# Optimization experiments

Measured on AMD Instinct MI355X. Metric: run time of the kernel, lower is better.

## Reference

```python
import jax, jax.numpy as jnp
import numpy as np

NC, NF = 64, 16
Z_NEAR, Z_FAR = 2.0, 6.0
EPS = 1e-5


def volume_integral(z_vals, sigmas, radiances):
    # z_vals/sigmas: (B,R,Z,1), radiances: (B,R,Z,F)
    d = z_vals[..., 1:, :] - z_vals[..., :-1, :]
    dists = jnp.concatenate([d, d[..., -1:, :]], axis=-2)            # (B,R,Z,1)
    alpha = 1.0 - jnp.exp(-jax.nn.relu(sigmas) * dists)
    alpha_shifted = jnp.concatenate(
        [jnp.ones_like(alpha[..., :1, :]), 1.0 - alpha + 1e-10], axis=-2)
    Ts = jnp.cumprod(alpha_shifted, axis=-2)                         # transmittance
    weights = alpha * Ts[..., :-1, :]                                # (B,R,Z,1)
    rgb = jnp.sum(weights * radiances, axis=-2)                      # (B,R,F)
    depth = jnp.sum(weights * z_vals, axis=-2)                       # (B,R,1)
    return rgb, depth, weights


def sample_pdf(bins, weights, u, eps=EPS):
    # bins: (N, S+1), weights: (N, S), u: (N, Nf) in [0,1)
    weights = weights + eps
    pdf = weights / jnp.sum(weights, -1, keepdims=True)
    cdf = jnp.cumsum(pdf, -1)
    cdf = jnp.concatenate([jnp.zeros_like(cdf[:, :1]), cdf], -1)     # (N, S+1)
    inds = jax.vmap(jnp.searchsorted)(cdf, u)                        # side='left' == torch default
    below = jnp.clip(inds - 1, 0, None)
    above = jnp.minimum(inds, weights.shape[-1])
    cdf_g0 = jnp.take_along_axis(cdf, below, 1)
    cdf_g1 = jnp.take_along_axis(cdf, above, 1)
    bins_g0 = jnp.take_along_axis(bins, below, 1)
    bins_g1 = jnp.take_along_axis(bins, above, 1)
    denom = cdf_g1 - cdf_g0
    denom = jnp.where(denom < eps, 1.0, denom)
    return bins_g0 + (u - cdf_g0) / denom * (bins_g1 - bins_g0)


def _render(ros, rds, w_sigma, w_feat, u):
    B, R, _ = ros.shape

    def rad(pts):
        return pts @ w_sigma, jax.nn.sigmoid(pts @ w_feat)

    # coarse stratified samples (lindisp=False)
    zl = jnp.linspace(0.0, 1.0, NC, dtype=ros.dtype)
    z_vals = Z_NEAR + (Z_FAR - Z_NEAR) * zl                          # (NC,)
    z_vals = jnp.broadcast_to(z_vals[None, None, :, None], (B, R, NC, 1))
    pts = ros[:, :, None, :] + rds[:, :, None, :] * z_vals           # (B,R,NC,3)
    sigma, feats = rad(pts)

    # coarse pass + importance resampling (no grad in original)
    _, _, weights = volume_integral(z_vals, sigma, feats)
    weights = jax.lax.stop_gradient(weights).reshape(B * R, NC)
    t = z_vals.reshape(B * R, NC)
    tm = 0.5 * (t[:, :-1] + t[:, 1:])                                # (N, NC-1)
    t_pdf = sample_pdf(tm, weights[:, 1:-1], u)                      # (N, NF)
    t_pdf = jax.lax.stop_gradient(t_pdf).reshape(B, R, NF)

    pts_fine = ros[:, :, None, :] + rds[:, :, None, :] * t_pdf[..., None]
    pts_all = jnp.concatenate([pts, pts_fine], axis=-2)              # (B,R,NC+NF,3)
    sigma_all, feats_all = rad(pts_all)

    # merge-sort coarse+fine by depth and gather
    z_all = jnp.concatenate([z_vals, t_pdf[..., None]], axis=-2)     # (B,R,Z,1)
    idx = jnp.argsort(z_all, axis=-2)
    z_all = jnp.take_along_axis(z_all, idx, axis=-2)
    sigma_all = jnp.take_along_axis(sigma_all, idx, axis=-2)
    feats_all = jnp.take_along_axis(
        feats_all, jnp.broadcast_to(idx, feats_all.shape), axis=-2)

    rgb, depth, weights = volume_integral(z_all, sigma_all, feats_all)
    return rgb, depth, weights


def setup_inputs() -> dict:
    key = jax.random.key(0)
    k = jax.random.split(key, 5)
    B, R = 8, 16384
    return {
        "ros": jax.random.normal(k[0], (B, R, 3), jnp.float32),
        "rds": jax.random.normal(k[1], (B, R, 3), jnp.float32),
        "w_sigma": jax.random.normal(k[2], (3, 1), jnp.float32),
        "w_feat": jax.random.normal(k[3], (3, 3), jnp.float32),
        "u": jax.random.uniform(k[4], (B * R, NF), jnp.float32),
    }


def reference(ros, rds, w_sigma, w_feat, u):
    return _render(ros, rds, w_sigma, w_feat, u)
```

## Files before the change

### kernel.cpp

```cpp
#include <hip/hip_runtime.h>

#define NCC 64
#define NFF 16
#define NZ  80
#define BLK 128
#define SLOTS 63

__device__ __forceinline__ float zc_of(int i) {
    return fmaf(4.0f, (float)i * (1.0f / 63.0f), 2.0f);
}
__device__ __forceinline__ float tm_of(int i) {
    return 0.5f * (zc_of(i) + zc_of(i + 1));
}
__device__ __forceinline__ float fast_rcp(float x) { return __builtin_amdgcn_rcpf(x); }

__global__ void __launch_bounds__(BLK, 2)
VolumeRenderer_16192026706363_kernel(const float* __restrict__ ros,
                                     const float* __restrict__ rds,
                                     const float* __restrict__ w_sigma,
                                     const float* __restrict__ w_feat,
                                     const float* __restrict__ u,
                                     float* __restrict__ out,
                                     int nrays)
{
    __shared__ float lds[BLK * SLOTS];
    const int tid = threadIdx.x;
    const int n = blockIdx.x * BLK + tid;
    float* my = &lds[tid * SLOTS];

    const float4* u4p = reinterpret_cast<const float4*>(u + (size_t)n * 16);
    float4 uq0 = u4p[0], uq1 = u4p[1], uq2 = u4p[2], uq3 = u4p[3];

    const float ro0 = ros[n * 3 + 0], ro1 = ros[n * 3 + 1], ro2 = ros[n * 3 + 2];
    const float rd0 = rds[n * 3 + 0], rd1 = rds[n * 3 + 1], rd2 = rds[n * 3 + 2];
    const float s0 = w_sigma[0], s1 = w_sigma[1], s2 = w_sigma[2];
    const float sgA = ro0 * s0 + ro1 * s1 + ro2 * s2;
    const float sgB = rd0 * s0 + rd1 * s1 + rd2 * s2;
    float fA[3], fB[3];
#pragma unroll
    for (int c = 0; c < 3; c++) {
        fA[c] = ro0 * w_feat[0 * 3 + c] + ro1 * w_feat[1 * 3 + c] + ro2 * w_feat[2 * 3 + c];
        fB[c] = rd0 * w_feat[0 * 3 + c] + rd1 * w_feat[1 * 3 + c] + rd2 * w_feat[2 * 3 + c];
    }

    const float LOG2E = 1.4426950408889634f;
    const float DIST  = 4.0f / 63.0f;
    const float K1    = -DIST * LOG2E;

    float T = 1.0f, cum = 0.0f;
    my[0] = 0.0f;
    {
        float e = exp2f(fmaxf(sgA + sgB * 2.0f, 0.0f) * K1);
        T = e + 1e-10f;
    }
    for (int i = 1; i <= 62; i++) {
        float sg = fmaf(sgB, zc_of(i), sgA);
        float e = exp2f(fmaxf(sg, 0.0f) * K1);
        float w = (1.0f - e) * T;
        cum += w + 1e-5f;
        my[i] = cum;
        T *= (e + 1e-10f);
    }
    const float S = cum;
    const float invS = 1.0f / S;

    float tv[16];
#pragma unroll
    for (int q = 0; q < 16; q++) {
        float uu;
        {
            float4 uq = (q < 4) ? uq0 : (q < 8) ? uq1 : (q < 12) ? uq2 : uq3;
            int r = q & 3;
            uu = (r == 0) ? uq.x : (r == 1) ? uq.y : (r == 2) ? uq.z : uq.w;
        }
        float us = uu * S;
        int lo = 0, hi = 63;
#pragma unroll
        for (int s = 0; s < 6; s++) {
            int mid = (lo + hi) >> 1;
            bool lt = (my[mid] < us);
            lo = lt ? mid + 1 : lo;
            hi = lt ? hi : mid;
        }
        int ind = lo;
        int below = (ind - 1 > 0) ? ind - 1 : 0;
        int above = (ind < 62) ? ind : 62;
        float c0 = my[below] * invS, c1 = my[above] * invS;
        float b0 = tm_of(below);
        float denom = c1 - c0;
        denom = (denom < 1e-5f) ? 1.0f : denom;
        float db = (4.0f / 63.0f) * (float)(above - below);
        tv[q] = fmaf((uu - c0) / denom, db, b0);
    }

#pragma unroll
    for (int k = 2; k <= 16; k <<= 1) {
#pragma unroll
        for (int j = k >> 1; j > 0; j >>= 1) {
#pragma unroll
            for (int i = 0; i < 16; i++) {
                int l = i ^ j;
                if (l > i) {
                    float a = tv[i], b = tv[l];
                    float mn = fminf(a, b), mx = fmaxf(a, b);
                    bool up = ((i & k) == 0);
                    tv[i] = up ? mn : mx;
                    tv[l] = up ? mx : mn;
                }
            }
        }
    }
#pragma unroll
    for (int i = 0; i < 16; i++) my[i] = tv[i];

    int ic = 0, jf = 0;
    float zch = 2.0f;
    float zfh = my[0];
    float T2 = 1.0f, acc0 = 0.0f, acc1 = 0.0f, acc2 = 0.0f, accd = 0.0f;

    auto pop = [&]() -> float {
        bool takeC = (zch <= zfh);
        float r = takeC ? zch : zfh;
        if (takeC) { ic++; zch = (ic < NCC) ? zc_of(ic) : 3.0e38f; }
        else       { jf++; zfh = (jf < NFF) ? my[jf] : 3.0e38f; }
        return r;
    };

    auto proc = [&](float z, float d) -> float {
        float sg = fmaf(sgB, z, sgA);
        float e = exp2f(fmaxf(sg, 0.0f) * d * (-LOG2E));
        float alpha = 1.0f - e;
        float w = alpha * T2;
        T2 *= (e + 1e-10f);
        float f0 = fast_rcp(1.0f + exp2f(fmaf(fB[0], z, fA[0]) * (-LOG2E)));
        float f1 = fast_rcp(1.0f + exp2f(fmaf(fB[1], z, fA[1]) * (-LOG2E)));
        float f2 = fast_rcp(1.0f + exp2f(fmaf(fB[2], z, fA[2]) * (-LOG2E)));
        acc0 = fmaf(w, f0, acc0);
        acc1 = fmaf(w, f1, acc1);
        acc2 = fmaf(w, f2, acc2);
        accd = fmaf(w, z, accd);
        return w;
    };

    float* wptr = out + (size_t)nrays * 4 + (size_t)n * NZ;
    float zprev = pop();
    float dlast = 0.0f;
    float wq[4];

    for (int g = 0; g < 19; g++) {
#pragma unroll
        for (int j = 0; j < 4; j++) {
            float z = pop();
            wq[j] = proc(zprev, z - zprev);
            zprev = z;
        }
        *reinterpret_cast<float4*>(wptr + g * 4) =
            make_float4(wq[0], wq[1], wq[2], wq[3]);
    }
#pragma unroll
    for (int j = 0; j < 3; j++) {
        float z = pop();
        dlast = z - zprev;
        wq[j] = proc(zprev, dlast);
        zprev = z;
    }
    wq[3] = proc(zprev, dlast);
    *reinterpret_cast<float4*>(wptr + 19 * 4) =
        make_float4(wq[0], wq[1], wq[2], wq[3]);

    out[(size_t)n * 3 + 0] = acc0;
    out[(size_t)n * 3 + 1] = acc1;
    out[(size_t)n * 3 + 2] = acc2;
    out[(size_t)nrays * 3 + n] = accd;
}

extern "C" void kernel_launch(void* const* d_in, const int* in_sizes, int n_in,
                              void* d_out, int out_size, void* d_ws, size_t ws_size,
                              hipStream_t stream) {
    const float* ros = (const float*)d_in[0];
    const float* rds = (const float*)d_in[1];
    const float* w_sigma = (const float*)d_in[2];
    const float* w_feat = (const float*)d_in[3];
    const float* u = (const float*)d_in[4];
    float* out = (float*)d_out;

    int nrays = in_sizes[0] / 3;
    int grid = nrays / BLK;
    VolumeRenderer_16192026706363_kernel<<<grid, BLK, 0, stream>>>(
        ros, rds, w_sigma, w_feat, u, out, nrays);
}
```

Measured before the change: 107.6 us.

## Replace serial scans and merge with register prefix scans and scatter-based merge

Swaps the serial transmittance and CDF recurrences for fully unrolled blocked prefix-product and prefix-sum scans held in registers, which shortens the dependency chains. The branchy coarse/fine merge loop is replaced by scattering each fine sample into an LDS slot computed from its coarse bin, followed by a branchless fill of the 80 sorted depths. The final pass then computes weights as differences of the prefix products and splits accumulation across two accumulator sets. Block size drops to 64 with a 79-float LDS stride. The large unrolled register arrays (g, c, z, pp) risk high VGPR pressure and spills, and the prefix-product form changes rounding slightly.

```diff
diff --git a/kernel.cpp b/kernel.cpp
--- a/kernel.cpp
+++ b/kernel.cpp
@@ -1,18 +1,68 @@
 #include <hip/hip_runtime.h>
 
+#define BLK 64
+#define STRIDE 79
 #define NCC 64
 #define NFF 16
 #define NZ  80
-#define BLK 128
-#define SLOTS 63
-
-__device__ __forceinline__ float zc_of(int i) {
-    return fmaf(4.0f, (float)i * (1.0f / 63.0f), 2.0f);
-}
-__device__ __forceinline__ float tm_of(int i) {
-    return 0.5f * (zc_of(i) + zc_of(i + 1));
-}
+
 __device__ __forceinline__ float fast_rcp(float x) { return __builtin_amdgcn_rcpf(x); }
+
+template<int N>
+__device__ __forceinline__ void prefix_mul(float* x) {
+#pragma unroll
+    for (int c = 0; c < N; c += 8) {
+#pragma unroll
+        for (int i = 1; i < 8; i++)
+            if (c + i < N) x[c + i] *= x[c + i - 1];
+    }
+    constexpr int G = (N + 7) / 8;
+    float t[G];
+#pragma unroll
+    for (int g = 0; g < G; g++) {
+        int e = 8 * g + 7; if (e > N - 1) e = N - 1;
+        t[g] = x[e];
+    }
+#pragma unroll
+    for (int sh = 1; sh < G; sh <<= 1) {
+#pragma unroll
+        for (int g = G - 1; g >= sh; --g) t[g] *= t[g - sh];
+    }
+#pragma unroll
+    for (int g = 1; g < G; g++) {
+#pragma unroll
+        for (int i = 0; i < 8; i++)
+            if (8 * g + i < N) x[8 * g + i] *= t[g - 1];
+    }
+}
+
+template<int N>
+__device__ __forceinline__ void prefix_add(float* x) {
+#pragma unroll
+    for (int c = 0; c < N; c += 8) {
+#pragma unroll
+        for (int i = 1; i < 8; i++)
+            if (c + i < N) x[c + i] += x[c + i - 1];
+    }
+    constexpr int G = (N + 7) / 8;
+    float t[G];
+#pragma unroll
+    for (int g = 0; g < G; g++) {
+        int e = 8 * g + 7; if (e > N - 1) e = N - 1;
+        t[g] = x[e];
+    }
+#pragma unroll
+    for (int sh = 1; sh < G; sh <<= 1) {
+#pragma unroll
+        for (int g = G - 1; g >= sh; --g) t[g] += t[g - sh];
+    }
+#pragma unroll
+    for (int g = 1; g < G; g++) {
+#pragma unroll
+        for (int i = 0; i < 8; i++)
+            if (8 * g + i < N) x[8 * g + i] += t[g - 1];
+    }
+}
 
 __global__ void __launch_bounds__(BLK, 2)
 VolumeRenderer_16192026706363_kernel(const float* __restrict__ ros,
@@ -23,17 +73,22 @@
                                      float* __restrict__ out,
                                      int nrays)
 {
-    __shared__ float lds[BLK * SLOTS];
+    __shared__ float lds[BLK * STRIDE];
     const int tid = threadIdx.x;
     const int n = blockIdx.x * BLK + tid;
-    float* my = &lds[tid * SLOTS];
+    float* my = &lds[tid * STRIDE];
+
+    const float LOG2E = 1.4426950408889634f;
+    const float NEGL2E = -LOG2E;
+    const float DIST = 4.0f / 63.0f;
+    const float K1 = -DIST * LOG2E;
 
     const float4* u4p = reinterpret_cast<const float4*>(u + (size_t)n * 16);
     float4 uq0 = u4p[0], uq1 = u4p[1], uq2 = u4p[2], uq3 = u4p[3];
-
     const float ro0 = ros[n * 3 + 0], ro1 = ros[n * 3 + 1], ro2 = ros[n * 3 + 2];
     const float rd0 = rds[n * 3 + 0], rd1 = rds[n * 3 + 1], rd2 = rds[n * 3 + 2];
     const float s0 = w_sigma[0], s1 = w_sigma[1], s2 = w_sigma[2];
+
     const float sgA = ro0 * s0 + ro1 * s1 + ro2 * s2;
     const float sgB = rd0 * s0 + rd1 * s1 + rd2 * s2;
     float fA[3], fB[3];
@@ -43,36 +98,37 @@
         fB[c] = rd0 * w_feat[0 * 3 + c] + rd1 * w_feat[1 * 3 + c] + rd2 * w_feat[2 * 3 + c];
     }
 
-    const float LOG2E = 1.4426950408889634f;
-    const float DIST  = 4.0f / 63.0f;
-    const float K1    = -DIST * LOG2E;
-
-    float T = 1.0f, cum = 0.0f;
+    float g[63];
+#pragma unroll
+    for (int i = 0; i < 63; i++) {
+        float zc = 2.0f + DIST * (float)i;
+        float sg = fmaf(sgB, zc, sgA);
+        g[i] = exp2f(fmaxf(sg, 0.0f) * K1) + 1e-10f;
+    }
+    prefix_mul<63>(g);
+
+    float c[63];
+    c[0] = 0.0f;
+#pragma unroll
+    for (int i = 1; i <= 62; i++) c[i] = (g[i - 1] - g[i]) + 1e-5f;
+    prefix_add<62>(c + 1);
+
     my[0] = 0.0f;
-    {
-        float e = exp2f(fmaxf(sgA + sgB * 2.0f, 0.0f) * K1);
-        T = e + 1e-10f;
-    }
-    for (int i = 1; i <= 62; i++) {
-        float sg = fmaf(sgB, zc_of(i), sgA);
-        float e = exp2f(fmaxf(sg, 0.0f) * K1);
-        float w = (1.0f - e) * T;
-        cum += w + 1e-5f;
-        my[i] = cum;
-        T *= (e + 1e-10f);
-    }
-    const float S = cum;
-    const float invS = 1.0f / S;
+#pragma unroll
+    for (int i = 1; i <= 62; i++) my[i] = c[i];
+    const float S = c[62];
+    const float invS = fast_rcp(S);
+
+    float uarr[16];
+    uarr[0]=uq0.x; uarr[1]=uq0.y; uarr[2]=uq0.z; uarr[3]=uq0.w;
+    uarr[4]=uq1.x; uarr[5]=uq1.y; uarr[6]=uq1.z; uarr[7]=uq1.w;
+    uarr[8]=uq2.x; uarr[9]=uq2.y; uarr[10]=uq2.z; uarr[11]=uq2.w;
+    uarr[12]=uq3.x; uarr[13]=uq3.y; uarr[14]=uq3.z; uarr[15]=uq3.w;
 
     float tv[16];
 #pragma unroll
     for (int q = 0; q < 16; q++) {
-        float uu;
-        {
-            float4 uq = (q < 4) ? uq0 : (q < 8) ? uq1 : (q < 12) ? uq2 : uq3;
-            int r = q & 3;
-            uu = (r == 0) ? uq.x : (r == 1) ? uq.y : (r == 2) ? uq.z : uq.w;
-        }
+        float uu = uarr[q];
         float us = uu * S;
         int lo = 0, hi = 63;
 #pragma unroll
@@ -86,11 +142,11 @@
         int below = (ind - 1 > 0) ? ind - 1 : 0;
         int above = (ind < 62) ? ind : 62;
         float c0 = my[below] * invS, c1 = my[above] * invS;
-        float b0 = tm_of(below);
+        float b0 = fmaf(DIST, (float)below, 2.0f + 0.5f * DIST);
         float denom = c1 - c0;
         denom = (denom < 1e-5f) ? 1.0f : denom;
-        float db = (4.0f / 63.0f) * (float)(above - below);
-        tv[q] = fmaf((uu - c0) / denom, db, b0);
+        float db = (above > below) ? DIST : 0.0f;
+        tv[q] = fmaf((uu - c0) * fast_rcp(denom), db, b0);
     }
 
 #pragma unroll
@@ -110,68 +166,79 @@
             }
         }
     }
-#pragma unroll
-    for (int i = 0; i < 16; i++) my[i] = tv[i];
-
-    int ic = 0, jf = 0;
-    float zch = 2.0f;
-    float zfh = my[0];
-    float T2 = 1.0f, acc0 = 0.0f, acc1 = 0.0f, acc2 = 0.0f, accd = 0.0f;
-
-    auto pop = [&]() -> float {
-        bool takeC = (zch <= zfh);
-        float r = takeC ? zch : zfh;
-        if (takeC) { ic++; zch = (ic < NCC) ? zc_of(ic) : 3.0e38f; }
-        else       { jf++; zfh = (jf < NFF) ? my[jf] : 3.0e38f; }
-        return r;
-    };
-
-    auto proc = [&](float z, float d) -> float {
-        float sg = fmaf(sgB, z, sgA);
-        float e = exp2f(fmaxf(sg, 0.0f) * d * (-LOG2E));
-        float alpha = 1.0f - e;
-        float w = alpha * T2;
-        T2 *= (e + 1e-10f);
-        float f0 = fast_rcp(1.0f + exp2f(fmaf(fB[0], z, fA[0]) * (-LOG2E)));
-        float f1 = fast_rcp(1.0f + exp2f(fmaf(fB[1], z, fA[1]) * (-LOG2E)));
-        float f2 = fast_rcp(1.0f + exp2f(fmaf(fB[2], z, fA[2]) * (-LOG2E)));
-        acc0 = fmaf(w, f0, acc0);
-        acc1 = fmaf(w, f1, acc1);
-        acc2 = fmaf(w, f2, acc2);
-        accd = fmaf(w, z, accd);
-        return w;
-    };
-
+
+#pragma unroll
+    for (int k = 0; k < 78; k++) my[k] = -1.0f;
+#pragma unroll
+    for (int j = 0; j < 16; j++) {
+        float x = (tv[j] - 2.0f) * 15.75f;
+        int L = (int)floorf(x) + 1;
+        L = (L < 1) ? 1 : (L > 63 ? 63 : L);
+        my[j + L - 1] = tv[j];
+    }
+
+    float z[NZ];
+    z[0] = 2.0f;
+    z[NZ - 1] = 6.0f;
+    {
+        float fc = 0.0f;
+#pragma unroll
+        for (int k = 1; k <= 78; k++) {
+            float s = my[k - 1];
+            bool fine = (s >= 0.0f);
+            float zc = fmaf(DIST, (float)k - fc, 2.0f);
+            z[k] = fine ? s : zc;
+            fc += fine ? 1.0f : 0.0f;
+        }
+    }
+
+    float pp[NZ];
+    float dl = 0.0f;
+#pragma unroll
+    for (int k = 0; k < NZ; k++) {
+        float d;
+        if (k < NZ - 1) { d = z[k + 1] - z[k]; dl = d; }
+        else d = dl;
+        float sg = fmaf(sgB, z[k], sgA);
+        pp[k] = exp2f(fmaxf(sg, 0.0f) * (d * NEGL2E)) + 1e-10f;
+    }
+    prefix_mul<NZ>(pp);
+
+    float a0 = 0.f, a1 = 0.f, a2 = 0.f, ad = 0.f;
+    float b0a = 0.f, b1a = 0.f, b2a = 0.f, bda = 0.f;
     float* wptr = out + (size_t)nrays * 4 + (size_t)n * NZ;
-    float zprev = pop();
-    float dlast = 0.0f;
-    float wq[4];
-
-    for (int g = 0; g < 19; g++) {
+#pragma unroll
+    for (int gq = 0; gq < 20; gq++) {
+        float wq[4];
 #pragma unroll
         for (int j = 0; j < 4; j++) {
-            float z = pop();
-            wq[j] = proc(zprev, z - zprev);
-            zprev = z;
-        }
-        *reinterpret_cast<float4*>(wptr + g * 4) =
+            int k = 4 * gq + j;
+            float prev = (k == 0) ? 1.0f : pp[k - 1];
+            float w = prev - pp[k];
+            float zk = z[k];
+            float e0 = exp2f(fmaf(fB[0], zk, fA[0]) * NEGL2E);
+            float e1 = exp2f(fmaf(fB[1], zk, fA[1]) * NEGL2E);
+            float e2 = exp2f(fmaf(fB[2], zk, fA[2]) * NEGL2E);
+            float f0 = fast_rcp(1.0f + e0);
+            float f1 = fast_rcp(1.0f + e1);
+            float f2 = fast_rcp(1.0f + e2);
+            if (j & 1) {
+                b0a = fmaf(w, f0, b0a); b1a = fmaf(w, f1, b1a);
+                b2a = fmaf(w, f2, b2a); bda = fmaf(w, zk, bda);
+            } else {
+                a0 = fmaf(w, f0, a0); a1 = fmaf(w, f1, a1);
+                a2 = fmaf(w, f2, a2); ad = fmaf(w, zk, ad);
+            }
+            wq[j] = w;
+        }
+        *reinterpret_cast<float4*>(wptr + 4 * gq) =
             make_float4(wq[0], wq[1], wq[2], wq[3]);
     }
-#pragma unroll
-    for (int j = 0; j < 3; j++) {
-        float z = pop();
-        dlast = z - zprev;
-        wq[j] = proc(zprev, dlast);
-        zprev = z;
-    }
-    wq[3] = proc(zprev, dlast);
-    *reinterpret_cast<float4*>(wptr + 19 * 4) =
-        make_float4(wq[0], wq[1], wq[2], wq[3]);
-
-    out[(size_t)n * 3 + 0] = acc0;
-    out[(size_t)n * 3 + 1] = acc1;
-    out[(size_t)n * 3 + 2] = acc2;
-    out[(size_t)nrays * 3 + n] = accd;
+
+    out[(size_t)n * 3 + 0] = a0 + b0a;
+    out[(size_t)n * 3 + 1] = a1 + b1a;
+    out[(size_t)n * 3 + 2] = a2 + b2a;
+    out[(size_t)nrays * 3 + n] = ad + bda;
 }
 
 extern "C" void kernel_launch(void* const* d_in, const int* in_sizes, int n_in,
```

Measured after the change: 108.2 us. Within noise of the previous version (+0.6%).
